# Performance work log

Hardware: AMD Instinct MI355X
Metric: run time of the kernel (lower is better)

## Reference

```python
import jax, jax.numpy as jnp
import numpy as np

B, V, I, O, G = 128, 1024, 512, 512, 16


def setup_inputs() -> dict:
    key = jax.random.key(0)
    kx, kg, kw, kb = jax.random.split(key, 4)
    x = jax.random.normal(kx, (B, V, I), dtype=jnp.float32)
    group_index = jax.random.randint(kg, (V,), 0, G, dtype=jnp.int64)
    weight = jax.random.normal(kw, (G, O, I), dtype=jnp.float32) * (1.0 / np.sqrt(I))
    bias = jax.random.normal(kb, (G, O), dtype=jnp.float32) * 0.01
    return {"x": x, "group_index": group_index, "weight": weight, "bias": bias}


def reference(x, group_index, weight, bias):
    # Gather per-node weights/bias (torch.index_select along group dim)
    w = weight[group_index]          # [V, O, I]
    b = bias[group_index]            # [V, O]
    # einsum '...VI,VOI->...VO' with leading batch dim b
    out = jnp.einsum('bvi,voi->bvo', x, w)  # [B, V, O]
    return out + b
```

## Files before the change

### kernel.cpp

```cpp
#include <hip/hip_runtime.h>
#include <stdint.h>

#define B_DIM 128
#define V_DIM 1024
#define I_DIM 512
#define O_DIM 512
#define G_DIM 16

#define TM 128
#define TN 128
#define BK 32
#define KSTEPS (I_DIM / BK)

typedef __bf16 bf16x8 __attribute__((ext_vector_type(8)));
typedef __bf16 bf16x4 __attribute__((ext_vector_type(4)));
typedef float  f32x4  __attribute__((ext_vector_type(4)));

#define GLOBAL_AS __attribute__((address_space(1)))
#define LDS_AS    __attribute__((address_space(3)))

__device__ __forceinline__ void dma16(const void* g, void* l) {
    __builtin_amdgcn_global_load_lds((const GLOBAL_AS uint32_t*)g,
                                     (LDS_AS uint32_t*)l, 16, 0, 0);
}

__device__ __forceinline__ bf16x8 cvt8(f32x4 lo, f32x4 hi) {
    bf16x8 r;
    r[0] = (__bf16)lo[0]; r[1] = (__bf16)lo[1]; r[2] = (__bf16)lo[2]; r[3] = (__bf16)lo[3];
    r[4] = (__bf16)hi[0]; r[5] = (__bf16)hi[1]; r[6] = (__bf16)hi[2]; r[7] = (__bf16)hi[3];
    return r;
}

__global__ __launch_bounds__(256) void convert_w(const float* __restrict__ src,
                                                 __bf16* __restrict__ dst) {
    const int i = blockIdx.x * 256 + threadIdx.x;
    float4 v = ((const float4*)src)[i];
    bf16x4 o;
    o[0] = (__bf16)v.x; o[1] = (__bf16)v.y; o[2] = (__bf16)v.z; o[3] = (__bf16)v.w;
    *(bf16x4*)&dst[(size_t)i * 4] = o;
}

__global__ __launch_bounds__(256, 4)
void glinear_mfma(const float* __restrict__ x,
                  const int*   __restrict__ gidx,
                  const __bf16* __restrict__ wb,
                  const float* __restrict__ bias,
                  float*       __restrict__ out) {
    const int v  = blockIdx.y;
    const int n0 = blockIdx.x * TN;
    const int g  = gidx[v];

    __shared__ float  lds_a[2][TM * BK];
    __shared__ __bf16 lds_b[TN * BK];

    const int tid  = threadIdx.x;
    const int lane = tid & 63;
    const int wave = tid >> 6;
    const int wm   = (wave & 1) * 64;
    const int wn   = (wave >> 1) * 64;
    const int fr   = lane & 15;
    const int c0   = lane >> 4;

    const int ar = lane >> 3;
    const int agc = (lane & 7) ^ ar;
    const float* aga[4];
#pragma unroll
    for (int j = 0; j < 4; ++j) {
        const int r = wave * 32 + j * 8 + ar;
        aga[j] = x + ((size_t)r * V_DIM + v) * I_DIM + agc * 4;
    }
    const int br = lane >> 2;
    const int bgc = (lane & 3) ^ ((lane >> 3) & 3);
    const __bf16* bga[2];
#pragma unroll
    for (int j = 0; j < 2; ++j) {
        const int r = wave * 32 + j * 16 + br;
        bga[j] = wb + ((size_t)(g * O_DIM + n0 + r)) * I_DIM + bgc * 8;
    }

    f32x4 acc[4][4];
    const f32x4 zero = {0.f, 0.f, 0.f, 0.f};
#pragma unroll
    for (int ms = 0; ms < 4; ++ms)
#pragma unroll
        for (int ns = 0; ns < 4; ++ns) acc[ms][ns] = zero;

#pragma unroll
    for (int j = 0; j < 4; ++j)
        dma16(aga[j], &lds_a[0][(wave * 32 + j * 8) * BK]);
#pragma unroll
    for (int j = 0; j < 2; ++j)
        dma16(bga[j], &lds_b[(wave * 32 + j * 16) * BK]);
    __syncthreads();

    const int ar7 = fr & 7;
    const int as0 = (2 * c0)     ^ ar7;
    const int as1 = (2 * c0 + 1) ^ ar7;
    const int bs  = c0 ^ ((fr >> 1) & 3);

    for (int kt = 0; kt < KSTEPS; ++kt) {
        const int cur = kt & 1;

        bf16x8 av[4], bv[4];
#pragma unroll
        for (int t = 0; t < 4; ++t) {
            const float* ab = &lds_a[cur][(wm + t * 16 + fr) * BK];
            f32x4 alo = *(const f32x4*)(ab + as0 * 4);
            f32x4 ahi = *(const f32x4*)(ab + as1 * 4);
            av[t] = cvt8(alo, ahi);
            bv[t] = *(const bf16x8*)&lds_b[(wn + t * 16 + fr) * BK + bs * 8];
        }
        __syncthreads();

        if (kt < KSTEPS - 1) {
#pragma unroll
            for (int j = 0; j < 4; ++j)
                dma16(aga[j] + (kt + 1) * BK, &lds_a[cur ^ 1][(wave * 32 + j * 8) * BK]);
#pragma unroll
            for (int j = 0; j < 2; ++j)
                dma16(bga[j] + (kt + 1) * BK, &lds_b[(wave * 32 + j * 16) * BK]);
        }

#pragma unroll
        for (int ms = 0; ms < 4; ++ms)
#pragma unroll
            for (int ns = 0; ns < 4; ++ns)
                acc[ms][ns] = __builtin_amdgcn_mfma_f32_16x16x32_bf16(
                    av[ms], bv[ns], acc[ms][ns], 0, 0, 0);

        __syncthreads();
    }

    const float* bptr = bias + (size_t)g * O_DIM + n0;
    float bvals[4];
#pragma unroll
    for (int ns = 0; ns < 4; ++ns) bvals[ns] = bptr[wn + ns * 16 + fr];

    const int rbase = (lane >> 4) * 4;
#pragma unroll
    for (int ms = 0; ms < 4; ++ms) {
#pragma unroll
        for (int r = 0; r < 4; ++r) {
            const int m = wm + ms * 16 + rbase + r;
            float* orow = out + ((size_t)m * V_DIM + v) * O_DIM + n0;
#pragma unroll
            for (int ns = 0; ns < 4; ++ns)
                orow[wn + ns * 16 + fr] = acc[ms][ns][r] + bvals[ns];
        }
    }
}

#define LDK 40
__device__ __forceinline__ __bf16 f2bf(float f) {
    unsigned u = __builtin_bit_cast(unsigned, f);
    u += 0x7fffu + ((u >> 16) & 1u);
    unsigned short h = (unsigned short)(u >> 16);
    return __builtin_bit_cast(__bf16, h);
}
__device__ __forceinline__ void cvt_store16(__bf16* dst, const float4* src) {
    bf16x8 lo, hi;
    lo[0] = f2bf(src[0].x); lo[1] = f2bf(src[0].y); lo[2] = f2bf(src[0].z); lo[3] = f2bf(src[0].w);
    lo[4] = f2bf(src[1].x); lo[5] = f2bf(src[1].y); lo[6] = f2bf(src[1].z); lo[7] = f2bf(src[1].w);
    hi[0] = f2bf(src[2].x); hi[1] = f2bf(src[2].y); hi[2] = f2bf(src[2].z); hi[3] = f2bf(src[2].w);
    hi[4] = f2bf(src[3].x); hi[5] = f2bf(src[3].y); hi[6] = f2bf(src[3].z); hi[7] = f2bf(src[3].w);
    *(bf16x8*)dst = lo; *(bf16x8*)(dst + 8) = hi;
}
__global__ __launch_bounds__(256, 2)
void glinear_fb(const float* __restrict__ x, const int* __restrict__ gidx,
                const float* __restrict__ w, const float* __restrict__ bias,
                float* __restrict__ out) {
    const int v = blockIdx.y, n0 = blockIdx.x * TN, g = gidx[v];
    __shared__ __bf16 lds_a[2][TM * LDK];
    __shared__ __bf16 lds_b[2][TN * LDK];
    const int tid = threadIdx.x, lane = tid & 63, wave = tid >> 6;
    const int wm = (wave & 1) * 64, wn = (wave >> 1) * 64;
    const int fr = lane & 15, kg = (lane >> 4) * 8;
    const int srow = tid >> 1, skh = (tid & 1) * 16;
    const float* xrow = x + ((size_t)srow * V_DIM + v) * I_DIM + skh;
    const float* wrow = w + (((size_t)g * O_DIM) + n0 + srow) * I_DIM + skh;
    const int soff = srow * LDK + skh;
    f32x4 acc[4][4];
    const f32x4 zero = {0.f, 0.f, 0.f, 0.f};
#pragma unroll
    for (int ms = 0; ms < 4; ++ms)
#pragma unroll
        for (int ns = 0; ns < 4; ++ns) acc[ms][ns] = zero;
    {
        float4 ax[4], bx[4];
#pragma unroll
        for (int i = 0; i < 4; ++i) { ax[i] = ((const float4*)xrow)[i]; bx[i] = ((const float4*)wrow)[i]; }
        cvt_store16(&lds_a[0][soff], ax); cvt_store16(&lds_b[0][soff], bx);
    }
    __syncthreads();
    for (int kt = 0; kt < KSTEPS; ++kt) {
        const int cur = kt & 1, nxt = cur ^ 1;
        float4 ax[4], bx[4];
        if (kt < KSTEPS - 1) {
            const float* xp = xrow + (kt + 1) * BK;
            const float* wp = wrow + (kt + 1) * BK;
#pragma unroll
            for (int i = 0; i < 4; ++i) { ax[i] = ((const float4*)xp)[i]; bx[i] = ((const float4*)wp)[i]; }
        }
        bf16x8 av[4], bv[4];
#pragma unroll
        for (int t = 0; t < 4; ++t) {
            av[t] = *(const bf16x8*)&lds_a[cur][(wm + t * 16 + fr) * LDK + kg];
            bv[t] = *(const bf16x8*)&lds_b[cur][(wn + t * 16 + fr) * LDK + kg];
        }
#pragma unroll
        for (int ms = 0; ms < 4; ++ms)
#pragma unroll
            for (int ns = 0; ns < 4; ++ns)
                acc[ms][ns] = __builtin_amdgcn_mfma_f32_16x16x32_bf16(av[ms], bv[ns], acc[ms][ns], 0, 0, 0);
        if (kt < KSTEPS - 1) { cvt_store16(&lds_a[nxt][soff], ax); cvt_store16(&lds_b[nxt][soff], bx); }
        __syncthreads();
    }
    const float* bptr = bias + (size_t)g * O_DIM + n0;
    float bvals[4];
#pragma unroll
    for (int ns = 0; ns < 4; ++ns) bvals[ns] = bptr[wn + ns * 16 + fr];
    const int rbase = (lane >> 4) * 4;
#pragma unroll
    for (int ms = 0; ms < 4; ++ms)
#pragma unroll
        for (int r = 0; r < 4; ++r) {
            const int m = wm + ms * 16 + rbase + r;
            float* orow = out + ((size_t)m * V_DIM + v) * O_DIM + n0;
#pragma unroll
            for (int ns = 0; ns < 4; ++ns) orow[wn + ns * 16 + fr] = acc[ms][ns][r] + bvals[ns];
        }
}

extern "C" void kernel_launch(void* const* d_in, const int* in_sizes, int n_in,
                              void* d_out, int out_size, void* d_ws, size_t ws_size,
                              hipStream_t stream) {
    const float* x    = (const float*)d_in[0];
    const int*   gidx = (const int*)d_in[1];
    const float* w    = (const float*)d_in[2];
    const float* bias = (const float*)d_in[3];
    float*       out  = (float*)d_out;

    const size_t w_elems = (size_t)G_DIM * O_DIM * I_DIM;
    const size_t need    = w_elems * sizeof(__bf16);

    if (ws_size >= need) {
        __bf16* wb = (__bf16*)d_ws;
        convert_w<<<(int)(w_elems / 4 / 256), 256, 0, stream>>>(w, wb);
        dim3 grid(O_DIM / TN, V_DIM);
        glinear_mfma<<<grid, 256, 0, stream>>>(x, gidx, wb, bias, out);
    } else {
        dim3 grid(O_DIM / TN, V_DIM);
        glinear_fb<<<grid, 256, 0, stream>>>(x, gidx, w, bias, out);
    }
}
```

Baseline: 639.7 us.

## Use full-O tiles per node with pre-packed swizzled bf16 weights

Each block now covers a whole node v with all 512 outputs, using 512 threads and an 8-wide N sub-tile per wave, so x rows are read from global memory once instead of four times. The weight conversion kernel now writes bf16 weights in a k-tile-major, pre-swizzled layout, so each K-step's B tile is one contiguous block that can be DMA'd straight into LDS. The A buffer drops from double to single buffering. The trade-offs are more accumulator registers, more LDS per block, fewer resident blocks, and less overlap between loads and MFMA.

```diff
diff --git a/kernel.cpp b/kernel.cpp
--- a/kernel.cpp
+++ b/kernel.cpp
@@ -8,9 +8,10 @@
 #define G_DIM 16
 
 #define TM 128
-#define TN 128
+#define TN 512
 #define BK 32
 #define KSTEPS (I_DIM / BK)
+#define TILE_ELEMS (O_DIM * BK)
 
 typedef __bf16 bf16x8 __attribute__((ext_vector_type(8)));
 typedef __bf16 bf16x4 __attribute__((ext_vector_type(4)));
@@ -31,66 +32,68 @@
     return r;
 }
 
-__global__ __launch_bounds__(256) void convert_w(const float* __restrict__ src,
-                                                 __bf16* __restrict__ dst) {
-    const int i = blockIdx.x * 256 + threadIdx.x;
-    float4 v = ((const float4*)src)[i];
-    bf16x4 o;
-    o[0] = (__bf16)v.x; o[1] = (__bf16)v.y; o[2] = (__bf16)v.z; o[3] = (__bf16)v.w;
-    *(bf16x4*)&dst[(size_t)i * 4] = o;
-}
-
-__global__ __launch_bounds__(256, 4)
+__global__ __launch_bounds__(256) void convert_w_packed(const float* __restrict__ src,
+                                                        __bf16* __restrict__ dst) {
+    const int cid  = blockIdx.x * 256 + threadIdx.x;
+    const int c    = cid & 63;
+    const int olin = cid >> 6;
+    const int o    = olin & (O_DIM - 1);
+    const int g    = olin >> 9;
+    const int kt   = c >> 2;
+    const int cc   = c & 3;
+    const int s    = cc ^ ((o >> 1) & 3);
+    const float4* sp = (const float4*)(src + (size_t)olin * I_DIM + c * 8);
+    float4 v0 = sp[0], v1 = sp[1];
+    bf16x8 r;
+    r[0] = (__bf16)v0.x; r[1] = (__bf16)v0.y; r[2] = (__bf16)v0.z; r[3] = (__bf16)v0.w;
+    r[4] = (__bf16)v1.x; r[5] = (__bf16)v1.y; r[6] = (__bf16)v1.z; r[7] = (__bf16)v1.w;
+    *(bf16x8*)&dst[((size_t)(g * KSTEPS + kt) * O_DIM + o) * BK + s * 8] = r;
+}
+
+__global__ __launch_bounds__(512, 2)
 void glinear_mfma(const float* __restrict__ x,
                   const int*   __restrict__ gidx,
                   const __bf16* __restrict__ wb,
                   const float* __restrict__ bias,
                   float*       __restrict__ out) {
-    const int v  = blockIdx.y;
-    const int n0 = blockIdx.x * TN;
-    const int g  = gidx[v];
-
-    __shared__ float  lds_a[2][TM * BK];
+    const int v = blockIdx.x;
+    const int g = gidx[v];
+
+    __shared__ float  lds_a[TM * BK];
     __shared__ __bf16 lds_b[TN * BK];
 
     const int tid  = threadIdx.x;
     const int lane = tid & 63;
     const int wave = tid >> 6;
     const int wm   = (wave & 1) * 64;
-    const int wn   = (wave >> 1) * 64;
+    const int wn   = (wave >> 1) * 128;
     const int fr   = lane & 15;
     const int c0   = lane >> 4;
 
-    const int ar = lane >> 3;
+    const int ar  = lane >> 3;
     const int agc = (lane & 7) ^ ar;
-    const float* aga[4];
-#pragma unroll
-    for (int j = 0; j < 4; ++j) {
-        const int r = wave * 32 + j * 8 + ar;
+    const float* aga[2];
+#pragma unroll
+    for (int j = 0; j < 2; ++j) {
+        const int r = wave * 16 + j * 8 + ar;
         aga[j] = x + ((size_t)r * V_DIM + v) * I_DIM + agc * 4;
     }
-    const int br = lane >> 2;
-    const int bgc = (lane & 3) ^ ((lane >> 3) & 3);
-    const __bf16* bga[2];
-#pragma unroll
-    for (int j = 0; j < 2; ++j) {
-        const int r = wave * 32 + j * 16 + br;
-        bga[j] = wb + ((size_t)(g * O_DIM + n0 + r)) * I_DIM + bgc * 8;
-    }
-
-    f32x4 acc[4][4];
+    const __bf16* btile = wb + (size_t)g * KSTEPS * TILE_ELEMS;
+
+    f32x4 acc[4][8];
     const f32x4 zero = {0.f, 0.f, 0.f, 0.f};
 #pragma unroll
     for (int ms = 0; ms < 4; ++ms)
 #pragma unroll
-        for (int ns = 0; ns < 4; ++ns) acc[ms][ns] = zero;
-
+        for (int ns = 0; ns < 8; ++ns) acc[ms][ns] = zero;
+
+#pragma unroll
+    for (int j = 0; j < 2; ++j)
+        dma16(aga[j], &lds_a[(wave * 16 + j * 8) * BK]);
 #pragma unroll
     for (int j = 0; j < 4; ++j)
-        dma16(aga[j], &lds_a[0][(wave * 32 + j * 8) * BK]);
-#pragma unroll
-    for (int j = 0; j < 2; ++j)
-        dma16(bga[j], &lds_b[(wave * 32 + j * 16) * BK]);
+        dma16(btile + (wave * 64 + j * 16) * BK + lane * 8,
+              &lds_b[(wave * 64 + j * 16) * BK]);
     __syncthreads();
 
     const int ar7 = fr & 7;
@@ -99,42 +102,45 @@
     const int bs  = c0 ^ ((fr >> 1) & 3);
 
     for (int kt = 0; kt < KSTEPS; ++kt) {
-        const int cur = kt & 1;
-
-        bf16x8 av[4], bv[4];
+        bf16x8 av[4], bv[8];
 #pragma unroll
         for (int t = 0; t < 4; ++t) {
-            const float* ab = &lds_a[cur][(wm + t * 16 + fr) * BK];
+            const float* ab = &lds_a[(wm + t * 16 + fr) * BK];
             f32x4 alo = *(const f32x4*)(ab + as0 * 4);
             f32x4 ahi = *(const f32x4*)(ab + as1 * 4);
             av[t] = cvt8(alo, ahi);
+        }
+#pragma unroll
+        for (int t = 0; t < 8; ++t)
             bv[t] = *(const bf16x8*)&lds_b[(wn + t * 16 + fr) * BK + bs * 8];
-        }
         __syncthreads();
 
         if (kt < KSTEPS - 1) {
 #pragma unroll
+            for (int j = 0; j < 2; ++j)
+                dma16(aga[j] + (kt + 1) * BK, &lds_a[(wave * 16 + j * 8) * BK]);
+            const __bf16* bt = btile + (size_t)(kt + 1) * TILE_ELEMS;
+#pragma unroll
             for (int j = 0; j < 4; ++j)
-                dma16(aga[j] + (kt + 1) * BK, &lds_a[cur ^ 1][(wave * 32 + j * 8) * BK]);
-#pragma unroll
-            for (int j = 0; j < 2; ++j)
-                dma16(bga[j] + (kt + 1) * BK, &lds_b[(wave * 32 + j * 16) * BK]);
+                dma16(bt + (wave * 64 + j * 16) * BK + lane * 8,
+                      &lds_b[(wave * 64 + j * 16) * BK]);
         }
 
 #pragma unroll
         for (int ms = 0; ms < 4; ++ms)
 #pragma unroll
-            for (int ns = 0; ns < 4; ++ns)
+            for (int ns = 0; ns < 8; ++ns)
                 acc[ms][ns] = __builtin_amdgcn_mfma_f32_16x16x32_bf16(
                     av[ms], bv[ns], acc[ms][ns], 0, 0, 0);
 
-        __syncthreads();
-    }
-
-    const float* bptr = bias + (size_t)g * O_DIM + n0;
-    float bvals[4];
-#pragma unroll
-    for (int ns = 0; ns < 4; ++ns) bvals[ns] = bptr[wn + ns * 16 + fr];
+        if (kt < KSTEPS - 1)
+            __syncthreads();
+    }
+
+    const float* bptr = bias + (size_t)g * O_DIM;
+    float bvals[8];
+#pragma unroll
+    for (int ns = 0; ns < 8; ++ns) bvals[ns] = bptr[wn + ns * 16 + fr];
 
     const int rbase = (lane >> 4) * 4;
 #pragma unroll
@@ -142,14 +148,15 @@
 #pragma unroll
         for (int r = 0; r < 4; ++r) {
             const int m = wm + ms * 16 + rbase + r;
-            float* orow = out + ((size_t)m * V_DIM + v) * O_DIM + n0;
-#pragma unroll
-            for (int ns = 0; ns < 4; ++ns)
+            float* orow = out + ((size_t)m * V_DIM + v) * O_DIM;
+#pragma unroll
+            for (int ns = 0; ns < 8; ++ns)
                 orow[wn + ns * 16 + fr] = acc[ms][ns][r] + bvals[ns];
         }
     }
 }
 
+#define FBTN 128
 #define LDK 40
 __device__ __forceinline__ __bf16 f2bf(float f) {
     unsigned u = __builtin_bit_cast(unsigned, f);
@@ -169,9 +176,9 @@
 void glinear_fb(const float* __restrict__ x, const int* __restrict__ gidx,
                 const float* __restrict__ w, const float* __restrict__ bias,
                 float* __restrict__ out) {
-    const int v = blockIdx.y, n0 = blockIdx.x * TN, g = gidx[v];
+    const int v = blockIdx.y, n0 = blockIdx.x * FBTN, g = gidx[v];
     __shared__ __bf16 lds_a[2][TM * LDK];
-    __shared__ __bf16 lds_b[2][TN * LDK];
+    __shared__ __bf16 lds_b[2][FBTN * LDK];
     const int tid = threadIdx.x, lane = tid & 63, wave = tid >> 6;
     const int wm = (wave & 1) * 64, wn = (wave >> 1) * 64;
     const int fr = lane & 15, kg = (lane >> 4) * 8;
@@ -245,11 +252,10 @@
 
     if (ws_size >= need) {
         __bf16* wb = (__bf16*)d_ws;
-        convert_w<<<(int)(w_elems / 4 / 256), 256, 0, stream>>>(w, wb);
-        dim3 grid(O_DIM / TN, V_DIM);
-        glinear_mfma<<<grid, 256, 0, stream>>>(x, gidx, wb, bias, out);
+        convert_w_packed<<<(int)(w_elems / 8 / 256), 256, 0, stream>>>(w, wb);
+        glinear_mfma<<<dim3(V_DIM), 512, 0, stream>>>(x, gidx, wb, bias, out);
     } else {
-        dim3 grid(O_DIM / TN, V_DIM);
+        dim3 grid(O_DIM / FBTN, V_DIM);
         glinear_fb<<<grid, 256, 0, stream>>>(x, gidx, w, bias, out);
     }
 }
```

After: 536.0 us. 16.2% less time.
